# Optimization experiments

Hardware: AMD Instinct MI355X
Metric: run time of the kernel (lower is better)

Reference implementation:

```python
import jax, jax.numpy as jnp
import numpy as np

N_HEADS = 32
N_KV_HEADS = 8
HEAD_DIM = 128
ROPE_THETA = 10000.0


def _rope_tables(T, dim, dtype):
    inv_freq = 1.0 / (ROPE_THETA ** (jnp.arange(0, dim, 2, dtype=jnp.float32) / dim))
    t = jnp.arange(T, dtype=jnp.float32)
    freqs = jnp.outer(t, inv_freq)            # [T, dim/2]
    emb = jnp.concatenate([freqs, freqs], -1) # [T, dim]
    return jnp.cos(emb).astype(dtype), jnp.sin(emb).astype(dtype)


def _rotate_half(x):
    x1, x2 = jnp.split(x, 2, axis=-1)
    return jnp.concatenate([-x2, x1], axis=-1)


def setup_inputs() -> dict:
    key = jax.random.key(0)
    ks = jax.random.split(key, 5)
    B, T, D = 1, 2048, 4096
    KV = N_KV_HEADS * HEAD_DIM
    s = 0.02
    return {
        "x": jax.random.normal(ks[0], (B, T, D), jnp.float32),
        "wq": jax.random.normal(ks[1], (D, D), jnp.float32) * s,
        "wk": jax.random.normal(ks[2], (D, KV), jnp.float32) * s,
        "wv": jax.random.normal(ks[3], (D, KV), jnp.float32) * s,
        "wo": jax.random.normal(ks[4], (D, D), jnp.float32) * s,
    }


def reference(x, wq, wk, wv, wo):
    B, T, D = x.shape
    n_rep = N_HEADS // N_KV_HEADS
    # projections -> [B, H, T, hd]
    q = (x @ wq).reshape(B, T, N_HEADS, HEAD_DIM).transpose(0, 2, 1, 3)
    k = (x @ wk).reshape(B, T, N_KV_HEADS, HEAD_DIM).transpose(0, 2, 1, 3)
    v = (x @ wv).reshape(B, T, N_KV_HEADS, HEAD_DIM).transpose(0, 2, 1, 3)
    cos, sin = _rope_tables(T, HEAD_DIM, x.dtype)  # [T, hd]
    cos = cos[None, None]  # [1,1,T,hd]
    sin = sin[None, None]
    q = q * cos + _rotate_half(q) * sin
    k = k * cos + _rotate_half(k) * sin
    # GQA: repeat_interleave kv heads
    k = jnp.repeat(k, n_rep, axis=1)
    v = jnp.repeat(v, n_rep, axis=1)
    scores = jnp.einsum("bhqd,bhkd->bhqk", q, k) / np.sqrt(HEAD_DIM).astype(x.dtype)
    causal = jnp.triu(jnp.ones((T, T), bool), k=1)
    scores = jnp.where(causal[None, None], jnp.asarray(-jnp.inf, scores.dtype), scores)
    attn = jax.nn.softmax(scores, axis=-1)
    out = jnp.einsum("bhqk,bhkd->bhqd", attn, v)
    out = out.transpose(0, 2, 1, 3).reshape(B, T, N_HEADS * HEAD_DIM)
    return out @ wo
```

## Files before the change

kernel.cpp:

```cpp
#include <hip/hip_runtime.h>
#include <hip/hip_bf16.h>
#include <cstdint>
#include <cmath>

typedef __bf16 bf16;
typedef __attribute__((ext_vector_type(8))) __bf16 bf16x8;
typedef __attribute__((ext_vector_type(4))) __bf16 bf16x4;
typedef __attribute__((ext_vector_type(4))) float f32x4;

#define T_SEQ   2048
#define D_MODEL 4096
#define KV_DIM  1024
#define NH      32
#define NKV     8
#define HD      128

__device__ __forceinline__ void gload16(const void* g, void* l) {
    __builtin_amdgcn_global_load_lds(
        (__attribute__((address_space(1))) void*)g,
        (__attribute__((address_space(3))) void*)l, 16, 0, 0);
}

__global__ void cvt_f32_bf16(const float* __restrict__ in, bf16* __restrict__ out, int n) {
    int i = (blockIdx.x * 256 + threadIdx.x) * 4;
    if (i >= n) return;
    float4 v = *(const float4*)(in + i);
    bf16x4 o = { (bf16)v.x, (bf16)v.y, (bf16)v.z, (bf16)v.w };
    *(bf16x4*)(out + i) = o;
}

__global__ void trans_f32_bf16(const float* __restrict__ in, bf16* __restrict__ out, int R, int C) {
    __shared__ float tile[32][33];
    int tc = C >> 5;
    int br = blockIdx.x / tc, bc = blockIdx.x % tc;
    int r0 = br << 5, c0 = bc << 5;
    int lr = threadIdx.x >> 5, lc = threadIdx.x & 31;
#pragma unroll
    for (int i = 0; i < 4; ++i)
        tile[lr + i * 8][lc] = in[(size_t)(r0 + lr + i * 8) * C + c0 + lc];
    __syncthreads();
#pragma unroll
    for (int i = 0; i < 4; ++i) {
        int oc = lr + i * 8;
        out[(size_t)(c0 + oc) * R + r0 + lc] = (bf16)tile[lc][oc];
    }
}

__global__ void trans_bf16(const bf16* __restrict__ in, bf16* __restrict__ out, int R, int C) {
    __shared__ bf16 tile[32][33];
    int tc = C >> 5;
    int br = blockIdx.x / tc, bc = blockIdx.x % tc;
    int r0 = br << 5, c0 = bc << 5;
    int lr = threadIdx.x >> 5, lc = threadIdx.x & 31;
#pragma unroll
    for (int i = 0; i < 4; ++i)
        tile[lr + i * 8][lc] = in[(size_t)(r0 + lr + i * 8) * C + c0 + lc];
    __syncthreads();
#pragma unroll
    for (int i = 0; i < 4; ++i) {
        int oc = lr + i * 8;
        out[(size_t)(c0 + oc) * R + r0 + lc] = tile[lc][oc];
    }
}

__global__ void rope_table(float* __restrict__ cosT, float* __restrict__ sinT) {
    int i = blockIdx.x * 256 + threadIdx.x;
    if (i >= T_SEQ * 64) return;
    int t = i >> 6, j = i & 63;
    float inv = powf(10000.0f, -(float)j / 64.0f);
    float ang = (float)t * inv;
    cosT[i] = cosf(ang);
    sinT[i] = sinf(ang);
}

__global__ void rope_apply(bf16* __restrict__ qk, const float* __restrict__ cosT,
                           const float* __restrict__ sinT, int H, int stride) {
    int i = blockIdx.x * 256 + threadIdx.x;
    if (i >= T_SEQ * H * 64) return;
    int j = i & 63;
    int h = (i >> 6) % H;
    int t = i / (64 * H);
    size_t base = (size_t)t * stride + h * HD;
    float a = (float)qk[base + j];
    float b = (float)qk[base + j + 64];
    float c = cosT[t * 64 + j], s = sinT[t * 64 + j];
    qk[base + j]      = (bf16)(a * c - b * s);
    qk[base + j + 64] = (bf16)(b * c + a * s);
}

template <int MODE>
__global__ __launch_bounds__(256, 3) void gemm_nt(const bf16* __restrict__ A,
                                                  const bf16* __restrict__ Bt,
                                                  void* __restrict__ O0, void* __restrict__ O1,
                                                  void* __restrict__ O2,
                                                  int M, int N, int K) {
    __shared__ bf16 ldsA[128 * 64];
    __shared__ bf16 ldsB[128 * 64];
    const int tiles_n = N >> 7;
    const int bm = blockIdx.x / tiles_n;
    const int bn = blockIdx.x % tiles_n;
    const int tid = threadIdx.x;
    const int lane = tid & 63;
    const int wid = tid >> 6;
    const int wr = wid >> 1, wc = wid & 1;
    const int l16 = lane & 15, l4 = lane >> 4;
    f32x4 acc[4][4] = {};
    const size_t row0 = (size_t)bm * 128, col0 = (size_t)bn * 128;
    const bf16* Abase = A + row0 * K;
    const bf16* Bbase = Bt + col0 * K;
    const int srow = wid * 8 + (lane >> 3);
    const int scol = (lane & 7) * 8;

    for (int k0 = 0; k0 < K; k0 += 64) {
#pragma unroll
        for (int c = 0; c < 4; ++c) {
            int r = c * 32 + srow;
            gload16(Abase + (size_t)r * K + k0 + scol, &ldsA[(c * 32 + wid * 8) * 64]);
            gload16(Bbase + (size_t)r * K + k0 + scol, &ldsB[(c * 32 + wid * 8) * 64]);
        }
        asm volatile("s_waitcnt vmcnt(0)" ::: "memory");
        __syncthreads();
#pragma unroll
        for (int kk = 0; kk < 2; ++kk) {
            bf16x8 af[4], bfr[4];
#pragma unroll
            for (int m = 0; m < 4; ++m)
                af[m] = *(const bf16x8*)&ldsA[(wr * 64 + m * 16 + l16) * 64 + kk * 32 + l4 * 8];
#pragma unroll
            for (int n = 0; n < 4; ++n)
                bfr[n] = *(const bf16x8*)&ldsB[(wc * 64 + n * 16 + l16) * 64 + kk * 32 + l4 * 8];
#pragma unroll
            for (int m = 0; m < 4; ++m)
#pragma unroll
                for (int n = 0; n < 4; ++n)
                    acc[m][n] = __builtin_amdgcn_mfma_f32_16x16x32_bf16(af[m], bfr[n], acc[m][n], 0, 0, 0);
        }
        __syncthreads();
    }
#pragma unroll
    for (int m = 0; m < 4; ++m)
#pragma unroll
        for (int n = 0; n < 4; ++n)
#pragma unroll
            for (int r = 0; r < 4; ++r) {
                size_t row = row0 + wr * 64 + m * 16 + l4 * 4 + r;
                size_t col = col0 + wc * 64 + n * 16 + l16;
                float v = acc[m][n][r];
                if (MODE == 1) {
                    ((float*)O0)[row * N + col] = v;
                } else if (MODE == 0) {
                    ((bf16*)O0)[row * N + col] = (bf16)v;
                } else {
                    if (col < 4096)
                        ((bf16*)O0)[row * 4096 + col] = (bf16)v;
                    else if (col < 5120)
                        ((bf16*)O1)[row * 1024 + (col - 4096)] = (bf16)v;
                    else
                        ((bf16*)O2)[row * 1024 + (col - 5120)] = (bf16)v;
                }
            }
}

__global__ __launch_bounds__(256, 3) void flash_attn(const bf16* __restrict__ Q,
                                                     const bf16* __restrict__ Kb,
                                                     const bf16* __restrict__ Vt,
                                                     bf16* __restrict__ ctx) {
    __shared__ bf16 ldsK[64 * 128];
    __shared__ bf16 ldsV[128 * 64];
    __shared__ bf16 ldsP[4][16 * 72];
    const int tid = threadIdx.x, lane = tid & 63, wid = tid >> 6;
    const int l16 = lane & 15, l4 = lane >> 4;
    const int kvh = blockIdx.x & 7;
    const int q0 = (127 - (int)(blockIdx.x >> 3)) * 16;
    const int h = kvh * 4 + wid;

    const bf16* qb = Q + (size_t)q0 * D_MODEL + h * HD;
    bf16x8 qf[4];
#pragma unroll
    for (int kk = 0; kk < 4; ++kk)
        qf[kk] = *(const bf16x8*)(qb + (size_t)l16 * D_MODEL + kk * 32 + l4 * 8);

    f32x4 acc[8] = {};
    float m_r[4], l_r[4];
#pragma unroll
    for (int r = 0; r < 4; ++r) { m_r[r] = -INFINITY; l_r[r] = 0.f; }
    const float scale = 0.08838834764831845f;
    bf16* Pw = ldsP[wid];
    const int nt = (q0 + 16 + 63) >> 6;

    const int krow = lane >> 4, kpg = lane & 15;
    const int vrow = lane >> 3, vpg = lane & 7;

    for (int t = 0; t < nt; ++t) {
        const int k0 = t * 64;
#pragma unroll
        for (int c = 0; c < 4; ++c) {
            int r = c * 16 + wid * 4 + krow;
            int g = kpg ^ (r & 15);
            gload16(Kb + (size_t)(k0 + r) * KV_DIM + kvh * HD + g * 8,
                    &ldsK[(c * 16 + wid * 4) * 128]);
        }
#pragma unroll
        for (int c = 0; c < 4; ++c) {
            int r = c * 32 + wid * 8 + vrow;
            int g = vpg ^ (r & 7);
            gload16(Vt + (size_t)(kvh * 128 + r) * T_SEQ + k0 + g * 8,
                    &ldsV[(c * 32 + wid * 8) * 64]);
        }
        asm volatile("s_waitcnt vmcnt(0)" ::: "memory");
        __syncthreads();

        f32x4 s[4] = {};
#pragma unroll
        for (int n = 0; n < 4; ++n) {
            int r = n * 16 + l16;
#pragma unroll
            for (int kk = 0; kk < 4; ++kk) {
                int pg = (kk * 4 + l4) ^ (r & 15);
                bf16x8 kf = *(const bf16x8*)&ldsK[r * 128 + pg * 8];
                s[n] = __builtin_amdgcn_mfma_f32_16x16x32_bf16(qf[kk], kf, s[n], 0, 0, 0);
            }
        }
#pragma unroll
        for (int n = 0; n < 4; ++n)
#pragma unroll
            for (int r = 0; r < 4; ++r) {
                int key = k0 + n * 16 + l16;
                int row = q0 + l4 * 4 + r;
                float sv = s[n][r] * scale;
                s[n][r] = (key > row) ? -INFINITY : sv;
            }
        float f[4];
#pragma unroll
        for (int r = 0; r < 4; ++r) {
            float v = fmaxf(fmaxf(s[0][r], s[1][r]), fmaxf(s[2][r], s[3][r]));
            v = fmaxf(v, __shfl_xor(v, 1));
            v = fmaxf(v, __shfl_xor(v, 2));
            v = fmaxf(v, __shfl_xor(v, 4));
            v = fmaxf(v, __shfl_xor(v, 8));
            float mn = fmaxf(m_r[r], v);
            f[r] = __expf(m_r[r] - mn);
            m_r[r] = mn;
        }
#pragma unroll
        for (int n = 0; n < 4; ++n)
#pragma unroll
            for (int r = 0; r < 4; ++r)
                s[n][r] = __expf(s[n][r] - m_r[r]);
#pragma unroll
        for (int r = 0; r < 4; ++r) {
            float ps = (s[0][r] + s[1][r]) + (s[2][r] + s[3][r]);
            ps += __shfl_xor(ps, 1);
            ps += __shfl_xor(ps, 2);
            ps += __shfl_xor(ps, 4);
            ps += __shfl_xor(ps, 8);
            l_r[r] = l_r[r] * f[r] + ps;
        }
#pragma unroll
        for (int n = 0; n < 8; ++n)
#pragma unroll
            for (int r = 0; r < 4; ++r)
                acc[n][r] *= f[r];
#pragma unroll
        for (int n = 0; n < 4; ++n)
#pragma unroll
            for (int r = 0; r < 4; ++r)
                Pw[(l4 * 4 + r) * 72 + n * 16 + l16] = (bf16)s[n][r];
        bf16x8 pf0 = *(const bf16x8*)&Pw[l16 * 72 + l4 * 8];
        bf16x8 pf1 = *(const bf16x8*)&Pw[l16 * 72 + 32 + l4 * 8];
#pragma unroll
        for (int n = 0; n < 8; ++n) {
            int r = n * 16 + l16;
            int pg0 = l4 ^ (r & 7);
            int pg1 = (4 + l4) ^ (r & 7);
            bf16x8 v0 = *(const bf16x8*)&ldsV[r * 64 + pg0 * 8];
            bf16x8 v1 = *(const bf16x8*)&ldsV[r * 64 + pg1 * 8];
            acc[n] = __builtin_amdgcn_mfma_f32_16x16x32_bf16(pf0, v0, acc[n], 0, 0, 0);
            acc[n] = __builtin_amdgcn_mfma_f32_16x16x32_bf16(pf1, v1, acc[n], 0, 0, 0);
        }
        __syncthreads();
    }
#pragma unroll
    for (int n = 0; n < 8; ++n)
#pragma unroll
        for (int r = 0; r < 4; ++r) {
            int row = q0 + l4 * 4 + r;
            ctx[(size_t)row * D_MODEL + h * HD + n * 16 + l16] = (bf16)(acc[n][r] / l_r[r]);
        }
}

extern "C" void kernel_launch(void* const* d_in, const int* in_sizes, int n_in,
                              void* d_out, int out_size, void* d_ws, size_t ws_size,
                              hipStream_t stream) {
    const float* x  = (const float*)d_in[0];
    const float* wq = (const float*)d_in[1];
    const float* wk = (const float*)d_in[2];
    const float* wv = (const float*)d_in[3];
    const float* wo = (const float*)d_in[4];
    float* out = (float*)d_out;

    char* ws = (char*)d_ws;
    size_t off = 0;
    auto alloc = [&](size_t bytes) {
        void* p = ws + off;
        off += (bytes + 255) & ~(size_t)255;
        return p;
    };
    bf16* xb    = (bf16*)alloc((size_t)T_SEQ * D_MODEL * 2);
    bf16* wqkvt = (bf16*)alloc((size_t)(D_MODEL + 2 * KV_DIM) * D_MODEL * 2);
    bf16* wot   = (bf16*)alloc((size_t)D_MODEL * D_MODEL * 2);
    bf16* q     = (bf16*)alloc((size_t)T_SEQ * D_MODEL * 2);
    bf16* k     = (bf16*)alloc((size_t)T_SEQ * KV_DIM * 2);
    bf16* v     = (bf16*)alloc((size_t)T_SEQ * KV_DIM * 2);
    bf16* vt    = (bf16*)alloc((size_t)KV_DIM * T_SEQ * 2);
    bf16* ctx   = (bf16*)alloc((size_t)T_SEQ * D_MODEL * 2);
    float* cosT = (float*)alloc((size_t)T_SEQ * 64 * 4);
    float* sinT = (float*)alloc((size_t)T_SEQ * 64 * 4);

    cvt_f32_bf16<<<(T_SEQ * D_MODEL) / 1024, 256, 0, stream>>>(x, xb, T_SEQ * D_MODEL);
    trans_f32_bf16<<<(D_MODEL / 32) * (D_MODEL / 32), 256, 0, stream>>>(wq, wqkvt, D_MODEL, D_MODEL);
    trans_f32_bf16<<<(D_MODEL / 32) * (KV_DIM / 32), 256, 0, stream>>>(
        wk, wqkvt + (size_t)D_MODEL * D_MODEL, D_MODEL, KV_DIM);
    trans_f32_bf16<<<(D_MODEL / 32) * (KV_DIM / 32), 256, 0, stream>>>(
        wv, wqkvt + (size_t)(D_MODEL + KV_DIM) * D_MODEL, D_MODEL, KV_DIM);
    trans_f32_bf16<<<(D_MODEL / 32) * (D_MODEL / 32), 256, 0, stream>>>(wo, wot, D_MODEL, D_MODEL);
    rope_table<<<(T_SEQ * 64) / 256, 256, 0, stream>>>(cosT, sinT);

    gemm_nt<2><<<(T_SEQ / 128) * ((D_MODEL + 2 * KV_DIM) / 128), 256, 0, stream>>>(
        xb, wqkvt, q, k, v, T_SEQ, D_MODEL + 2 * KV_DIM, D_MODEL);

    rope_apply<<<(T_SEQ * NH * 64) / 256, 256, 0, stream>>>(q, cosT, sinT, NH, D_MODEL);
    rope_apply<<<(T_SEQ * NKV * 64) / 256, 256, 0, stream>>>(k, cosT, sinT, NKV, KV_DIM);

    trans_bf16<<<(T_SEQ / 32) * (KV_DIM / 32), 256, 0, stream>>>(v, vt, T_SEQ, KV_DIM);

    flash_attn<<<1024, 256, 0, stream>>>(q, k, vt, ctx);

    gemm_nt<1><<<(T_SEQ / 128) * (D_MODEL / 128), 256, 0, stream>>>(
        ctx, wot, out, nullptr, nullptr, T_SEQ, D_MODEL, D_MODEL);
}
```

Baseline: 549.3 us.

## Double-buffer flash attention, fuse Q RoPE, merge weight transposes, swizzle GEMM blocks

Flash attention now processes 32 query rows per block with double-buffered K/V LDS tiles, issuing the next tile's loads before computing the current one, and uses s_setprio around MFMA sections. Q RoPE is applied inside the attention kernel, which removes a separate rope_apply pass over Q. The four weight transpose launches are merged into one, and GEMM block indices are remapped across groups of eight to change which tiles run concurrently and improve cache locality. Larger per-block work halves the attention grid and lowers occupancy (launch bounds drop from 3 to 2 blocks per SM), which may hurt latency hiding.

New measurement: 571.0 us. 1.04x slower.

```diff
diff --git a/kernel.cpp b/kernel.cpp
--- a/kernel.cpp
+++ b/kernel.cpp
@@ -29,20 +29,29 @@
     *(bf16x4*)(out + i) = o;
 }
 
-__global__ void trans_f32_bf16(const float* __restrict__ in, bf16* __restrict__ out, int R, int C) {
+__global__ void trans_weights(const float* __restrict__ wq, const float* __restrict__ wk,
+                              const float* __restrict__ wv, const float* __restrict__ wo,
+                              bf16* __restrict__ wqkvt, bf16* __restrict__ wot) {
     __shared__ float tile[32][33];
+    int b = blockIdx.x;
+    const float* src; bf16* dst; int C;
+    if (b < 16384)      { src = wq; dst = wqkvt;                           C = 4096; }
+    else if (b < 20480) { src = wk; dst = wqkvt + (size_t)4096 * 4096;     C = 1024; b -= 16384; }
+    else if (b < 24576) { src = wv; dst = wqkvt + (size_t)5120 * 4096;     C = 1024; b -= 20480; }
+    else                { src = wo; dst = wot;                             C = 4096; b -= 24576; }
+    const int R = 4096;
     int tc = C >> 5;
-    int br = blockIdx.x / tc, bc = blockIdx.x % tc;
+    int br = b / tc, bc = b % tc;
     int r0 = br << 5, c0 = bc << 5;
     int lr = threadIdx.x >> 5, lc = threadIdx.x & 31;
 #pragma unroll
     for (int i = 0; i < 4; ++i)
-        tile[lr + i * 8][lc] = in[(size_t)(r0 + lr + i * 8) * C + c0 + lc];
+        tile[lr + i * 8][lc] = src[(size_t)(r0 + lr + i * 8) * C + c0 + lc];
     __syncthreads();
 #pragma unroll
     for (int i = 0; i < 4; ++i) {
         int oc = lr + i * 8;
-        out[(size_t)(c0 + oc) * R + r0 + lc] = (bf16)tile[lc][oc];
+        dst[(size_t)(c0 + oc) * R + r0 + lc] = (bf16)tile[lc][oc];
     }
 }
 
@@ -97,8 +106,10 @@
     __shared__ bf16 ldsA[128 * 64];
     __shared__ bf16 ldsB[128 * 64];
     const int tiles_n = N >> 7;
-    const int bm = blockIdx.x / tiles_n;
-    const int bn = blockIdx.x % tiles_n;
+    const int cpx = gridDim.x >> 3;
+    const int swz = (blockIdx.x & 7) * cpx + (blockIdx.x >> 3);
+    const int bm = swz / tiles_n;
+    const int bn = swz % tiles_n;
     const int tid = threadIdx.x;
     const int lane = tid & 63;
     const int wid = tid >> 6;
@@ -161,132 +172,190 @@
             }
 }
 
-__global__ __launch_bounds__(256, 3) void flash_attn(const bf16* __restrict__ Q,
+__global__ __launch_bounds__(256, 2) void flash_attn(const bf16* __restrict__ Q,
                                                      const bf16* __restrict__ Kb,
                                                      const bf16* __restrict__ Vt,
+                                                     const float* __restrict__ cosT,
+                                                     const float* __restrict__ sinT,
                                                      bf16* __restrict__ ctx) {
-    __shared__ bf16 ldsK[64 * 128];
-    __shared__ bf16 ldsV[128 * 64];
+    __shared__ bf16 ldsK[2][64 * 128];
+    __shared__ bf16 ldsV[2][128 * 64];
     __shared__ bf16 ldsP[4][16 * 72];
     const int tid = threadIdx.x, lane = tid & 63, wid = tid >> 6;
     const int l16 = lane & 15, l4 = lane >> 4;
     const int kvh = blockIdx.x & 7;
-    const int q0 = (127 - (int)(blockIdx.x >> 3)) * 16;
+    const int i = blockIdx.x >> 3;
+    const int chunk = (i < 32) ? (63 - i) : (i - 32);
+    const int q0 = chunk * 32;
     const int h = kvh * 4 + wid;
 
-    const bf16* qb = Q + (size_t)q0 * D_MODEL + h * HD;
-    bf16x8 qf[4];
-#pragma unroll
-    for (int kk = 0; kk < 4; ++kk)
-        qf[kk] = *(const bf16x8*)(qb + (size_t)l16 * D_MODEL + kk * 32 + l4 * 8);
-
-    f32x4 acc[8] = {};
-    float m_r[4], l_r[4];
-#pragma unroll
-    for (int r = 0; r < 4; ++r) { m_r[r] = -INFINITY; l_r[r] = 0.f; }
+    bf16x8 qf[2][4];
+#pragma unroll
+    for (int hh = 0; hh < 2; ++hh) {
+        const int trow = q0 + hh * 16 + l16;
+        const bf16* qb = Q + (size_t)trow * D_MODEL + h * HD;
+        bf16x8 raw[4];
+#pragma unroll
+        for (int kk = 0; kk < 4; ++kk)
+            raw[kk] = *(const bf16x8*)(qb + kk * 32 + l4 * 8);
+#pragma unroll
+        for (int kk = 0; kk < 2; ++kk) {
+            const float* cb = cosT + trow * 64 + kk * 32 + l4 * 8;
+            const float* sb = sinT + trow * 64 + kk * 32 + l4 * 8;
+            f32x4 c0 = *(const f32x4*)cb, c1 = *(const f32x4*)(cb + 4);
+            f32x4 s0 = *(const f32x4*)sb, s1 = *(const f32x4*)(sb + 4);
+#pragma unroll
+            for (int e = 0; e < 8; ++e) {
+                float c = (e < 4) ? c0[e] : c1[e - 4];
+                float s = (e < 4) ? s0[e] : s1[e - 4];
+                float a = (float)raw[kk][e], b = (float)raw[kk + 2][e];
+                qf[hh][kk][e]     = (bf16)(a * c - b * s);
+                qf[hh][kk + 2][e] = (bf16)(b * c + a * s);
+            }
+        }
+    }
+
+    f32x4 acc[2][8] = {};
+    float m_r[2][4], l_r[2][4];
+#pragma unroll
+    for (int hh = 0; hh < 2; ++hh)
+#pragma unroll
+        for (int r = 0; r < 4; ++r) { m_r[hh][r] = -INFINITY; l_r[hh][r] = 0.f; }
     const float scale = 0.08838834764831845f;
     bf16* Pw = ldsP[wid];
-    const int nt = (q0 + 16 + 63) >> 6;
+    const int nt = (q0 >> 6) + 1;
 
     const int krow = lane >> 4, kpg = lane & 15;
     const int vrow = lane >> 3, vpg = lane & 7;
-
-    for (int t = 0; t < nt; ++t) {
-        const int k0 = t * 64;
+    auto stage = [&](int buf, int t) {
+        const int k0s = t * 64;
 #pragma unroll
         for (int c = 0; c < 4; ++c) {
             int r = c * 16 + wid * 4 + krow;
             int g = kpg ^ (r & 15);
-            gload16(Kb + (size_t)(k0 + r) * KV_DIM + kvh * HD + g * 8,
-                    &ldsK[(c * 16 + wid * 4) * 128]);
+            gload16(Kb + (size_t)(k0s + r) * KV_DIM + kvh * HD + g * 8,
+                    &ldsK[buf][(c * 16 + wid * 4) * 128]);
         }
 #pragma unroll
         for (int c = 0; c < 4; ++c) {
             int r = c * 32 + wid * 8 + vrow;
             int g = vpg ^ (r & 7);
-            gload16(Vt + (size_t)(kvh * 128 + r) * T_SEQ + k0 + g * 8,
-                    &ldsV[(c * 32 + wid * 8) * 64]);
-        }
-        asm volatile("s_waitcnt vmcnt(0)" ::: "memory");
-        __syncthreads();
-
-        f32x4 s[4] = {};
+            gload16(Vt + (size_t)(kvh * 128 + r) * T_SEQ + k0s + g * 8,
+                    &ldsV[buf][(c * 32 + wid * 8) * 64]);
+        }
+    };
+
+    stage(0, 0);
+    asm volatile("s_waitcnt vmcnt(0)" ::: "memory");
+    __syncthreads();
+
+    for (int t = 0; t < nt; ++t) {
+        const int cur = t & 1;
+        const int k0 = t * 64;
+        if (t + 1 < nt) stage(cur ^ 1, t + 1);
+
+        f32x4 s[2][4] = {};
+        const bf16* Kl = ldsK[cur];
+        __builtin_amdgcn_s_setprio(1);
 #pragma unroll
         for (int n = 0; n < 4; ++n) {
             int r = n * 16 + l16;
 #pragma unroll
             for (int kk = 0; kk < 4; ++kk) {
                 int pg = (kk * 4 + l4) ^ (r & 15);
-                bf16x8 kf = *(const bf16x8*)&ldsK[r * 128 + pg * 8];
-                s[n] = __builtin_amdgcn_mfma_f32_16x16x32_bf16(qf[kk], kf, s[n], 0, 0, 0);
-            }
-        }
-#pragma unroll
-        for (int n = 0; n < 4; ++n)
+                bf16x8 kf = *(const bf16x8*)&Kl[r * 128 + pg * 8];
+                s[0][n] = __builtin_amdgcn_mfma_f32_16x16x32_bf16(qf[0][kk], kf, s[0][n], 0, 0, 0);
+                s[1][n] = __builtin_amdgcn_mfma_f32_16x16x32_bf16(qf[1][kk], kf, s[1][n], 0, 0, 0);
+            }
+        }
+        __builtin_amdgcn_s_setprio(0);
+
+#pragma unroll
+        for (int hh = 0; hh < 2; ++hh) {
+#pragma unroll
+            for (int n = 0; n < 4; ++n)
+#pragma unroll
+                for (int r = 0; r < 4; ++r) {
+                    int key = k0 + n * 16 + l16;
+                    int row = q0 + hh * 16 + l4 * 4 + r;
+                    float sv = s[hh][n][r] * scale;
+                    s[hh][n][r] = (key > row) ? -INFINITY : sv;
+                }
+            float f[4];
 #pragma unroll
             for (int r = 0; r < 4; ++r) {
-                int key = k0 + n * 16 + l16;
-                int row = q0 + l4 * 4 + r;
-                float sv = s[n][r] * scale;
-                s[n][r] = (key > row) ? -INFINITY : sv;
-            }
-        float f[4];
-#pragma unroll
-        for (int r = 0; r < 4; ++r) {
-            float v = fmaxf(fmaxf(s[0][r], s[1][r]), fmaxf(s[2][r], s[3][r]));
-            v = fmaxf(v, __shfl_xor(v, 1));
-            v = fmaxf(v, __shfl_xor(v, 2));
-            v = fmaxf(v, __shfl_xor(v, 4));
-            v = fmaxf(v, __shfl_xor(v, 8));
-            float mn = fmaxf(m_r[r], v);
-            f[r] = __expf(m_r[r] - mn);
-            m_r[r] = mn;
-        }
-#pragma unroll
-        for (int n = 0; n < 4; ++n)
-#pragma unroll
-            for (int r = 0; r < 4; ++r)
-                s[n][r] = __expf(s[n][r] - m_r[r]);
-#pragma unroll
-        for (int r = 0; r < 4; ++r) {
-            float ps = (s[0][r] + s[1][r]) + (s[2][r] + s[3][r]);
-            ps += __shfl_xor(ps, 1);
-            ps += __shfl_xor(ps, 2);
-            ps += __shfl_xor(ps, 4);
-            ps += __shfl_xor(ps, 8);
-            l_r[r] = l_r[r] * f[r] + ps;
-        }
-#pragma unroll
-        for (int n = 0; n < 8; ++n)
-#pragma unroll
-            for (int r = 0; r < 4; ++r)
-                acc[n][r] *= f[r];
-#pragma unroll
-        for (int n = 0; n < 4; ++n)
-#pragma unroll
-            for (int r = 0; r < 4; ++r)
-                Pw[(l4 * 4 + r) * 72 + n * 16 + l16] = (bf16)s[n][r];
-        bf16x8 pf0 = *(const bf16x8*)&Pw[l16 * 72 + l4 * 8];
-        bf16x8 pf1 = *(const bf16x8*)&Pw[l16 * 72 + 32 + l4 * 8];
+                float v = fmaxf(fmaxf(s[hh][0][r], s[hh][1][r]), fmaxf(s[hh][2][r], s[hh][3][r]));
+                v = fmaxf(v, __shfl_xor(v, 1));
+                v = fmaxf(v, __shfl_xor(v, 2));
+                v = fmaxf(v, __shfl_xor(v, 4));
+                v = fmaxf(v, __shfl_xor(v, 8));
+                float mn = fmaxf(m_r[hh][r], v);
+                f[r] = __expf(m_r[hh][r] - mn);
+                m_r[hh][r] = mn;
+            }
+#pragma unroll
+            for (int n = 0; n < 4; ++n)
+#pragma unroll
+                for (int r = 0; r < 4; ++r)
+                    s[hh][n][r] = __expf(s[hh][n][r] - m_r[hh][r]);
+#pragma unroll
+            for (int r = 0; r < 4; ++r) {
+                float ps = (s[hh][0][r] + s[hh][1][r]) + (s[hh][2][r] + s[hh][3][r]);
+                ps += __shfl_xor(ps, 1);
+                ps += __shfl_xor(ps, 2);
+                ps += __shfl_xor(ps, 4);
+                ps += __shfl_xor(ps, 8);
+                l_r[hh][r] = l_r[hh][r] * f[r] + ps;
+            }
+#pragma unroll
+            for (int n = 0; n < 8; ++n)
+#pragma unroll
+                for (int r = 0; r < 4; ++r)
+                    acc[hh][n][r] *= f[r];
+        }
+
+        bf16x8 pf[2][2];
+#pragma unroll
+        for (int hh = 0; hh < 2; ++hh) {
+#pragma unroll
+            for (int n = 0; n < 4; ++n)
+#pragma unroll
+                for (int r = 0; r < 4; ++r)
+                    Pw[(l4 * 4 + r) * 72 + n * 16 + l16] = (bf16)s[hh][n][r];
+            pf[hh][0] = *(const bf16x8*)&Pw[l16 * 72 + l4 * 8];
+            pf[hh][1] = *(const bf16x8*)&Pw[l16 * 72 + 32 + l4 * 8];
+        }
+
+        const bf16* Vl = ldsV[cur];
+        __builtin_amdgcn_s_setprio(1);
 #pragma unroll
         for (int n = 0; n < 8; ++n) {
             int r = n * 16 + l16;
             int pg0 = l4 ^ (r & 7);
             int pg1 = (4 + l4) ^ (r & 7);
-            bf16x8 v0 = *(const bf16x8*)&ldsV[r * 64 + pg0 * 8];
-            bf16x8 v1 = *(const bf16x8*)&ldsV[r * 64 + pg1 * 8];
-            acc[n] = __builtin_amdgcn_mfma_f32_16x16x32_bf16(pf0, v0, acc[n], 0, 0, 0);
-            acc[n] = __builtin_amdgcn_mfma_f32_16x16x32_bf16(pf1, v1, acc[n], 0, 0, 0);
-        }
+            bf16x8 v0 = *(const bf16x8*)&Vl[r * 64 + pg0 * 8];
+            bf16x8 v1 = *(const bf16x8*)&Vl[r * 64 + pg1 * 8];
+            acc[0][n] = __builtin_amdgcn_mfma_f32_16x16x32_bf16(pf[0][0], v0, acc[0][n], 0, 0, 0);
+            acc[0][n] = __builtin_amdgcn_mfma_f32_16x16x32_bf16(pf[0][1], v1, acc[0][n], 0, 0, 0);
+            acc[1][n] = __builtin_amdgcn_mfma_f32_16x16x32_bf16(pf[1][0], v0, acc[1][n], 0, 0, 0);
+            acc[1][n] = __builtin_amdgcn_mfma_f32_16x16x32_bf16(pf[1][1], v1, acc[1][n], 0, 0, 0);
+        }
+        __builtin_amdgcn_s_setprio(0);
+
+        asm volatile("s_waitcnt vmcnt(0)" ::: "memory");
         __syncthreads();
     }
-#pragma unroll
-    for (int n = 0; n < 8; ++n)
-#pragma unroll
-        for (int r = 0; r < 4; ++r) {
-            int row = q0 + l4 * 4 + r;
-            ctx[(size_t)row * D_MODEL + h * HD + n * 16 + l16] = (bf16)(acc[n][r] / l_r[r]);
-        }
+
+#pragma unroll
+    for (int hh = 0; hh < 2; ++hh)
+#pragma unroll
+        for (int n = 0; n < 8; ++n)
+#pragma unroll
+            for (int r = 0; r < 4; ++r) {
+                int row = q0 + hh * 16 + l4 * 4 + r;
+                ctx[(size_t)row * D_MODEL + h * HD + n * 16 + l16] =
+                    (bf16)(acc[hh][n][r] / l_r[hh][r]);
+            }
 }
 
 extern "C" void kernel_launch(void* const* d_in, const int* in_sizes, int n_in,
@@ -318,23 +387,17 @@
     float* sinT = (float*)alloc((size_t)T_SEQ * 64 * 4);
 
     cvt_f32_bf16<<<(T_SEQ * D_MODEL) / 1024, 256, 0, stream>>>(x, xb, T_SEQ * D_MODEL);
-    trans_f32_bf16<<<(D_MODEL / 32) * (D_MODEL / 32), 256, 0, stream>>>(wq, wqkvt, D_MODEL, D_MODEL);
-    trans_f32_bf16<<<(D_MODEL / 32) * (KV_DIM / 32), 256, 0, stream>>>(
-        wk, wqkvt + (size_t)D_MODEL * D_MODEL, D_MODEL, KV_DIM);
-    trans_f32_bf16<<<(D_MODEL / 32) * (KV_DIM / 32), 256, 0, stream>>>(
-        wv, wqkvt + (size_t)(D_MODEL + KV_DIM) * D_MODEL, D_MODEL, KV_DIM);
-    trans_f32_bf16<<<(D_MODEL / 32) * (D_MODEL / 32), 256, 0, stream>>>(wo, wot, D_MODEL, D_MODEL);
+    trans_weights<<<40960, 256, 0, stream>>>(wq, wk, wv, wo, wqkvt, wot);
     rope_table<<<(T_SEQ * 64) / 256, 256, 0, stream>>>(cosT, sinT);
 
     gemm_nt<2><<<(T_SEQ / 128) * ((D_MODEL + 2 * KV_DIM) / 128), 256, 0, stream>>>(
         xb, wqkvt, q, k, v, T_SEQ, D_MODEL + 2 * KV_DIM, D_MODEL);
 
-    rope_apply<<<(T_SEQ * NH * 64) / 256, 256, 0, stream>>>(q, cosT, sinT, NH, D_MODEL);
     rope_apply<<<(T_SEQ * NKV * 64) / 256, 256, 0, stream>>>(k, cosT, sinT, NKV, KV_DIM);
 
     trans_bf16<<<(T_SEQ / 32) * (KV_DIM / 32), 256, 0, stream>>>(v, vt, T_SEQ, KV_DIM);
 
-    flash_attn<<<1024, 256, 0, stream>>>(q, k, vt, ctx);
+    flash_attn<<<512, 256, 0, stream>>>(q, k, vt, cosT, sinT, ctx);
 
     gemm_nt<1><<<(T_SEQ / 128) * (D_MODEL / 128), 256, 0, stream>>>(
         ctx, wot, out, nullptr, nullptr, T_SEQ, D_MODEL, D_MODEL);
```
